# Kernel tuning notes

Measured on AMD Instinct MI355X. Metric: run time of the kernel, lower is better.

Reference implementation:

```python
import jax, jax.numpy as jnp
import numpy as np

B, S, HIDDEN = 4, 2048, 1024
NUM_EXPERTS = 8
TOP_K = 4
EPS = 1e-6


def setup_inputs() -> dict:
    key = jax.random.key(0)
    k0, k1, k2 = jax.random.split(key, 3)
    x = jax.random.normal(k0, (B, S, HIDDEN), dtype=jnp.float32)
    Wg = jax.random.normal(k1, (HIDDEN, NUM_EXPERTS), dtype=jnp.float32) * 0.02
    bg = jnp.zeros((NUM_EXPERTS,), dtype=jnp.float32)
    W = jax.random.normal(k2, (NUM_EXPERTS, HIDDEN, HIDDEN), dtype=jnp.float32) * 0.02
    b = jnp.zeros((NUM_EXPERTS, HIDDEN), dtype=jnp.float32)
    return {"x": x, "Wg": Wg, "bg": bg, "W": W, "b": b}


def reference(x, Wg, bg, W, b):
    Bb, Ss, D = x.shape
    xf = x.reshape(-1, D)                       # [T, D]
    T = xf.shape[0]

    # --- router ---
    router_logits = xf @ Wg + bg                # [T, E]
    router_probs = jax.nn.softmax(router_logits, axis=-1)
    top_k_probs, top_k_indices = jax.lax.top_k(router_probs, TOP_K)  # [T, K]
    top_k_weights = top_k_probs / (top_k_probs.sum(axis=-1, keepdims=True) + EPS)
    expert_mask = jax.nn.one_hot(top_k_indices, NUM_EXPERTS, dtype=jnp.float32).sum(axis=1)  # [T, E]

    # --- experts: original computes every expert on every token then masks;
    # same math expressed as one batched GEMM + gather ---
    all_out = jnp.einsum('td,edf->etf', xf, W) + b[:, None, :]  # [E, T, D]
    sel = all_out[top_k_indices.T, jnp.arange(T)[None, :]]      # [K, T, D]
    moe_output = jnp.einsum('tk,ktd->td', top_k_weights, sel).reshape(Bb, Ss, D)

    # --- load-balancing aux loss ---
    aux_loss = jnp.dot(expert_mask.mean(axis=0), router_probs.mean(axis=0)) * NUM_EXPERTS
    return moe_output, aux_loss
```

## Files before the change

kernel.cpp:

```cpp
#include <hip/hip_runtime.h>
#include <hip/hip_bf16.h>

#define T_TOK 8192
#define DH    1024
#define NE    8
#define TK    4

typedef unsigned short u16;
typedef __bf16 bf16x8 __attribute__((ext_vector_type(8)));
typedef float  f32x4  __attribute__((ext_vector_type(4)));

__device__ __forceinline__ u16 f2b(float f) {
    union { float f; unsigned u; } v; v.f = f;
    unsigned u = v.u;
    u += 0x7FFFu + ((u >> 16) & 1u);
    return (u16)(u >> 16);
}
__device__ __forceinline__ float b2f(u16 h) {
    union { unsigned u; float f; } v; v.u = ((unsigned)h) << 16;
    return v.f;
}
__device__ __forceinline__ void glds16(const u16* g, u16* l) {
    __builtin_amdgcn_global_load_lds((const __attribute__((address_space(1))) void*)g,
                                     (__attribute__((address_space(3))) void*)l, 16, 0, 0);
}

__global__ __launch_bounds__(256) void cast_w_kernel(const float* __restrict__ W,
                                                     u16* __restrict__ wbt) {
    __shared__ float tile[32][33];
    const int e  = blockIdx.z;
    const int d0 = blockIdx.y * 32;
    const int f0 = blockIdx.x * 32;
    const float* src = W + ((size_t)e << 20);
    for (int r = threadIdx.y; r < 32; r += 8)
        tile[r][threadIdx.x] = src[(size_t)(d0 + r) * DH + f0 + threadIdx.x];
    __syncthreads();
    u16* dst = wbt + ((size_t)e << 20);
    for (int r = threadIdx.y; r < 32; r += 8)
        dst[(size_t)(f0 + r) * DH + d0 + threadIdx.x] = f2b(tile[threadIdx.x][r]);
}

__global__ __launch_bounds__(512) void router_kernel(
    const float* __restrict__ x, const float* __restrict__ Wg, const float* __restrict__ bg,
    u16* __restrict__ xb,
    int* __restrict__ bucket_tok, float* __restrict__ bucket_w,
    int* __restrict__ tk_e, float* __restrict__ tk_w,
    int* __restrict__ cnt, float* __restrict__ probsum)
{
    __shared__ int   lcnt[NE];
    __shared__ float lprob[NE];
    __shared__ int   gbase[NE];
    const int tid = threadIdx.x;
    const int wv = tid >> 6, lane = tid & 63;
    const int t = blockIdx.x * 8 + wv;
    if (tid < NE) { lcnt[tid] = 0; lprob[tid] = 0.f; }
    __syncthreads();

    float a[NE] = {};
    {
        const float* xr = x + (size_t)t * DH;
        u16* xbr = xb + (size_t)t * DH;
        #pragma unroll
        for (int it = 0; it < 4; it++) {
            const int d = it * 256 + lane * 4;
            const float4 v = *(const float4*)(xr + d);
            ushort4 o;
            o.x = f2b(v.x); o.y = f2b(v.y); o.z = f2b(v.z); o.w = f2b(v.w);
            *(ushort4*)(xbr + d) = o;
            const float* wr = Wg + d * NE;
            #pragma unroll
            for (int e = 0; e < NE; e++)
                a[e] += v.x * wr[e] + v.y * wr[NE + e] + v.z * wr[2 * NE + e] + v.w * wr[3 * NE + e];
        }
    }
    #pragma unroll
    for (int e = 0; e < NE; e++) {
        float v = a[e];
        #pragma unroll
        for (int off = 32; off > 0; off >>= 1) v += __shfl_down(v, off);
        a[e] = v;
    }

    int idx4[TK]; float w4[TK]; int off4[TK];
    if (lane == 0) {
        float logits[NE], probs[NE];
        float mx = -1e30f;
        #pragma unroll
        for (int e = 0; e < NE; e++) { logits[e] = a[e] + bg[e]; mx = fmaxf(mx, logits[e]); }
        float Z = 0.f;
        #pragma unroll
        for (int e = 0; e < NE; e++) { probs[e] = expf(logits[e] - mx); Z += probs[e]; }
        const float rZ = 1.f / Z;
        #pragma unroll
        for (int e = 0; e < NE; e++) probs[e] *= rZ;

        float rem[NE];
        #pragma unroll
        for (int e = 0; e < NE; e++) rem[e] = probs[e];
        float s4 = 0.f;
        #pragma unroll
        for (int k = 0; k < TK; k++) {
            int best = 0; float bv = rem[0];
            #pragma unroll
            for (int e = 1; e < NE; e++) if (rem[e] > bv) { bv = rem[e]; best = e; }
            idx4[k] = best; w4[k] = bv; s4 += bv; rem[best] = -1e30f;
        }
        const float rs = 1.f / (s4 + 1e-6f);
        #pragma unroll
        for (int k = 0; k < TK; k++) {
            w4[k] *= rs;
            tk_e[t * TK + k] = idx4[k];
            tk_w[t * TK + k] = w4[k];
            off4[k] = atomicAdd(&lcnt[idx4[k]], 1);
        }
        #pragma unroll
        for (int e = 0; e < NE; e++) atomicAdd(&lprob[e], probs[e]);
    }
    __syncthreads();
    if (tid < NE) {
        gbase[tid] = atomicAdd(&cnt[tid], lcnt[tid]);
        atomicAdd(&probsum[tid], lprob[tid]);
    }
    __syncthreads();
    if (lane == 0) {
        #pragma unroll
        for (int k = 0; k < TK; k++) {
            const int e = idx4[k];
            const int slot = gbase[e] + off4[k];
            bucket_tok[e * T_TOK + slot] = (t << 2) | k;
            bucket_w[e * T_TOK + slot]   = w4[k];
        }
    }
}

__global__ __launch_bounds__(256) void moe_gemm_kernel(
    const u16* __restrict__ xb, const u16* __restrict__ wbt,
    const int* __restrict__ bucket_tok, const float* __restrict__ bucket_w,
    const int* __restrict__ cnt, u16* __restrict__ y)
{
    const int e  = blockIdx.z;
    const int M  = cnt[e];
    const int m0 = blockIdx.y * 128;
    if (m0 >= M) return;
    const int n0 = blockIdx.x * 128;

    __shared__ u16 As[128 * 32];
    __shared__ u16 Bs[128 * 32];
    __shared__ int   s_tok[128];
    __shared__ float s_w[128];

    const int tid  = threadIdx.x;
    const int lane = tid & 63;
    const int wave = tid >> 6;

    if (tid < 128) {
        const int slot = m0 + tid;
        if (slot < M) {
            s_tok[tid] = bucket_tok[e * T_TOK + slot];
            s_w[tid]   = bucket_w[e * T_TOK + slot];
        } else { s_tok[tid] = -1; s_w[tid] = 0.f; }
    }
    __syncthreads();

    const int l4 = lane >> 2;
    const int c8 = (lane & 3) * 8;
    const int r0 = (2 * wave) * 16 + l4;
    const int r1 = r0 + 16;
    const int t0 = s_tok[r0], t1 = s_tok[r1];
    const u16* gA0 = xb + (size_t)(t0 >= 0 ? (t0 >> 2) : 0) * DH + c8;
    const u16* gA1 = xb + (size_t)(t1 >= 0 ? (t1 >> 2) : 0) * DH + c8;
    const u16* gB0 = wbt + ((size_t)e << 20) + (size_t)(n0 + r0) * DH + c8;
    const u16* gB1 = gB0 + (size_t)16 * DH;
    u16* lA0 = &As[(2 * wave)     * 512];
    u16* lA1 = &As[(2 * wave + 1) * 512];
    u16* lB0 = &Bs[(2 * wave)     * 512];
    u16* lB1 = &Bs[(2 * wave + 1) * 512];

    const int mrow = (wave >> 1) * 64;
    const int ncol = (wave & 1) * 64;
    const int fr   = lane & 15;
    const int fq   = (lane >> 4) * 8;

    f32x4 acc[4][4] = {};

    for (int k0 = 0; k0 < DH; k0 += 32) {
        glds16(gA0 + k0, lA0);
        glds16(gA1 + k0, lA1);
        glds16(gB0 + k0, lB0);
        glds16(gB1 + k0, lB1);
        __syncthreads();
        bf16x8 af[4], bfv[4];
        #pragma unroll
        for (int i = 0; i < 4; i++)
            af[i] = *(const bf16x8*)&As[(mrow + i * 16 + fr) * 32 + fq];
        #pragma unroll
        for (int j = 0; j < 4; j++)
            bfv[j] = *(const bf16x8*)&Bs[(ncol + j * 16 + fr) * 32 + fq];
        #pragma unroll
        for (int i = 0; i < 4; i++)
            #pragma unroll
            for (int j = 0; j < 4; j++)
                acc[i][j] = __builtin_amdgcn_mfma_f32_16x16x32_bf16(af[i], bfv[j], acc[i][j], 0, 0, 0);
        __syncthreads();
    }

    const int cl = lane & 15;
    const int rb = (lane >> 4) * 4;
    #pragma unroll
    for (int i = 0; i < 4; i++) {
        #pragma unroll
        for (int r = 0; r < 4; r++) {
            const int srow = mrow + i * 16 + rb + r;
            const int tok = s_tok[srow];
            if (tok < 0) continue;
            const float w = s_w[srow];
            u16* yr = y + (size_t)tok * DH + (n0 + ncol + cl);
            #pragma unroll
            for (int j = 0; j < 4; j++)
                yr[j * 16] = f2b(acc[i][j][r] * w);
        }
    }
}

__global__ __launch_bounds__(256) void combine_kernel(
    const u16* __restrict__ y, const int* __restrict__ tk_e, const float* __restrict__ tk_w,
    const float* __restrict__ bexp,
    const int* __restrict__ cnt, const float* __restrict__ probsum,
    float* __restrict__ out, float* __restrict__ out_aux)
{
    const int t = blockIdx.x;
    const int c = threadIdx.x * 4;
    if (t == 0 && threadIdx.x == 0) {
        float s = 0.f;
        for (int e = 0; e < NE; e++) s += (float)cnt[e] * probsum[e];
        out_aux[0] = s * (float)NE / ((float)T_TOK * (float)T_TOK);
    }
    float o0 = 0.f, o1 = 0.f, o2 = 0.f, o3 = 0.f;
    #pragma unroll
    for (int k = 0; k < TK; k++) {
        const int e   = tk_e[t * TK + k];
        const float w = tk_w[t * TK + k];
        const ushort4 yv = *(const ushort4*)(y + ((size_t)(t * TK + k)) * DH + c);
        const float4  bv = *(const float4*)(bexp + (size_t)e * DH + c);
        o0 += b2f(yv.x) + w * bv.x;
        o1 += b2f(yv.y) + w * bv.y;
        o2 += b2f(yv.z) + w * bv.z;
        o3 += b2f(yv.w) + w * bv.w;
    }
    float4 ov = {o0, o1, o2, o3};
    *(float4*)(out + (size_t)t * DH + c) = ov;
}

extern "C" void kernel_launch(void* const* d_in, const int* in_sizes, int n_in,
                              void* d_out, int out_size, void* d_ws, size_t ws_size,
                              hipStream_t stream)
{
    const float* x  = (const float*)d_in[0];
    const float* Wg = (const float*)d_in[1];
    const float* bg = (const float*)d_in[2];
    const float* W  = (const float*)d_in[3];
    const float* b  = (const float*)d_in[4];
    float* out = (float*)d_out;

    char* ws = (char*)d_ws;
    u16*   xb         = (u16*)(ws);
    u16*   wbt        = (u16*)(ws + 16777216);
    u16*   y          = (u16*)(ws + 33554432);
    int*   bucket_tok = (int*)(ws + 100663296);
    float* bucket_w   = (float*)(ws + 100925440);
    int*   tk_e       = (int*)(ws + 101187584);
    float* tk_w       = (float*)(ws + 101318656);
    int*   cnt        = (int*)(ws + 101449728);
    float* probsum    = (float*)(ws + 101449760);

    hipMemsetAsync(cnt, 0, 64, stream);

    cast_w_kernel<<<dim3(32, 32, NE), dim3(32, 8, 1), 0, stream>>>(W, wbt);
    router_kernel<<<1024, 512, 0, stream>>>(x, Wg, bg, xb, bucket_tok, bucket_w, tk_e, tk_w, cnt, probsum);
    moe_gemm_kernel<<<dim3(8, 64, NE), 256, 0, stream>>>(xb, wbt, bucket_tok, bucket_w, cnt, y);
    combine_kernel<<<8192, 256, 0, stream>>>(y, tk_e, tk_w, b, cnt, probsum, out, out + (size_t)T_TOK * DH);
}
```

Baseline: 262.7 us.

## Fuse weight cast and router into one prep kernel; swizzle GEMM LDS

```diff
diff --git a/kernel.cpp b/kernel.cpp
--- a/kernel.cpp
+++ b/kernel.cpp
@@ -25,34 +25,51 @@
                                      (__attribute__((address_space(3))) void*)l, 16, 0, 0);
 }
 
-__global__ __launch_bounds__(256) void cast_w_kernel(const float* __restrict__ W,
-                                                     u16* __restrict__ wbt) {
-    __shared__ float tile[32][33];
-    const int e  = blockIdx.z;
-    const int d0 = blockIdx.y * 32;
-    const int f0 = blockIdx.x * 32;
-    const float* src = W + ((size_t)e << 20);
-    for (int r = threadIdx.y; r < 32; r += 8)
-        tile[r][threadIdx.x] = src[(size_t)(d0 + r) * DH + f0 + threadIdx.x];
-    __syncthreads();
-    u16* dst = wbt + ((size_t)e << 20);
-    for (int r = threadIdx.y; r < 32; r += 8)
-        dst[(size_t)(f0 + r) * DH + d0 + threadIdx.x] = f2b(tile[threadIdx.x][r]);
-}
-
-__global__ __launch_bounds__(512) void router_kernel(
+__global__ __launch_bounds__(256) void prep_kernel(
     const float* __restrict__ x, const float* __restrict__ Wg, const float* __restrict__ bg,
-    u16* __restrict__ xb,
+    const float* __restrict__ W,
+    u16* __restrict__ xb, u16* __restrict__ wbt,
     int* __restrict__ bucket_tok, float* __restrict__ bucket_w,
     int* __restrict__ tk_e, float* __restrict__ tk_w,
     int* __restrict__ cnt, float* __restrict__ probsum)
 {
+    const int bid = blockIdx.x;
+    const int tid = threadIdx.x;
+
+    if (bid < 2048) {
+        __shared__ float tile[64][65];
+        const int e = bid >> 8, rem = bid & 255;
+        const int d0 = (rem >> 4) << 6, f0 = (rem & 15) << 6;
+        const int rr = tid >> 4, cc = (tid & 15) << 2;
+        const float* src = W + ((size_t)e << 20) + (size_t)d0 * DH + f0;
+        #pragma unroll
+        for (int i = 0; i < 4; i++) {
+            const float4 v = *(const float4*)(src + (size_t)(i * 16 + rr) * DH + cc);
+            tile[i * 16 + rr][cc]     = v.x;
+            tile[i * 16 + rr][cc + 1] = v.y;
+            tile[i * 16 + rr][cc + 2] = v.z;
+            tile[i * 16 + rr][cc + 3] = v.w;
+        }
+        __syncthreads();
+        u16* dst = wbt + ((size_t)e << 20) + (size_t)f0 * DH + d0;
+        #pragma unroll
+        for (int i = 0; i < 4; i++) {
+            const int orow = i * 16 + rr;
+            ushort4 o;
+            o.x = f2b(tile[cc][orow]);
+            o.y = f2b(tile[cc + 1][orow]);
+            o.z = f2b(tile[cc + 2][orow]);
+            o.w = f2b(tile[cc + 3][orow]);
+            *(ushort4*)(dst + (size_t)orow * DH + cc) = o;
+        }
+        return;
+    }
+
     __shared__ int   lcnt[NE];
     __shared__ float lprob[NE];
     __shared__ int   gbase[NE];
-    const int tid = threadIdx.x;
     const int wv = tid >> 6, lane = tid & 63;
-    const int t = blockIdx.x * 8 + wv;
+    const int t = (bid - 2048) * 4 + wv;
     if (tid < NE) { lcnt[tid] = 0; lprob[tid] = 0.f; }
     __syncthreads();
 
@@ -94,16 +111,16 @@
         #pragma unroll
         for (int e = 0; e < NE; e++) probs[e] *= rZ;
 
-        float rem[NE];
-        #pragma unroll
-        for (int e = 0; e < NE; e++) rem[e] = probs[e];
+        float rem2[NE];
+        #pragma unroll
+        for (int e = 0; e < NE; e++) rem2[e] = probs[e];
         float s4 = 0.f;
         #pragma unroll
         for (int k = 0; k < TK; k++) {
-            int best = 0; float bv = rem[0];
+            int best = 0; float bv = rem2[0];
             #pragma unroll
-            for (int e = 1; e < NE; e++) if (rem[e] > bv) { bv = rem[e]; best = e; }
-            idx4[k] = best; w4[k] = bv; s4 += bv; rem[best] = -1e30f;
+            for (int e = 1; e < NE; e++) if (rem2[e] > bv) { bv = rem2[e]; best = e; }
+            idx4[k] = best; w4[k] = bv; s4 += bv; rem2[best] = -1e30f;
         }
         const float rs = 1.f / (s4 + 1e-6f);
         #pragma unroll
@@ -163,7 +180,8 @@
     __syncthreads();
 
     const int l4 = lane >> 2;
-    const int c8 = (lane & 3) * 8;
+    const int gch = (lane & 3) ^ (l4 & 3) ^ ((l4 >> 2) & 3);
+    const int c8 = gch * 8;
     const int r0 = (2 * wave) * 16 + l4;
     const int r1 = r0 + 16;
     const int t0 = s_tok[r0], t1 = s_tok[r1];
@@ -179,7 +197,7 @@
     const int mrow = (wave >> 1) * 64;
     const int ncol = (wave & 1) * 64;
     const int fr   = lane & 15;
-    const int fq   = (lane >> 4) * 8;
+    const int fq   = (((lane >> 4) ^ (fr & 3) ^ ((fr >> 2) & 3))) * 8;
 
     f32x4 acc[4][4] = {};
 
@@ -275,8 +293,8 @@
 
     hipMemsetAsync(cnt, 0, 64, stream);
 
-    cast_w_kernel<<<dim3(32, 32, NE), dim3(32, 8, 1), 0, stream>>>(W, wbt);
-    router_kernel<<<1024, 512, 0, stream>>>(x, Wg, bg, xb, bucket_tok, bucket_w, tk_e, tk_w, cnt, probsum);
+    prep_kernel<<<4096, 256, 0, stream>>>(x, Wg, bg, W, xb, wbt,
+                                          bucket_tok, bucket_w, tk_e, tk_w, cnt, probsum);
     moe_gemm_kernel<<<dim3(8, 64, NE), 256, 0, stream>>>(xb, wbt, bucket_tok, bucket_w, cnt, y);
     combine_kernel<<<8192, 256, 0, stream>>>(y, tk_e, tk_w, b, cnt, probsum, out, out + (size_t)T_TOK * DH);
 }
```

Result: slower. 275.2 us (+4.7%).
